# Optimization experiments

Hardware: AMD Instinct MI355X
Metric: run time of the kernel (lower is better)

## Reference

```python
import jax, jax.numpy as jnp
import numpy as np

B, N, PS = 8, 2048, 32
P = N // PS          # 64 patches
D, MLP, DEPTH, H, DH = 1024, 2048, 6, 8, 64
INNER = H * DH       # 512
K = 20
EPS = 1e-5


def setup_inputs() -> dict:
    key = jax.random.key(0)
    ks = jax.random.split(key, 16)
    r = lambda i, shape: jax.random.normal(ks[i], shape, dtype=jnp.float32) * 0.02
    return {
        "x": jax.random.normal(ks[0], (B, N, 3), dtype=jnp.float32),
        "x_pos_embed": r(1, (B, P + 1, D)),
        "w1": r(2, (64, 6)),   "g1": jnp.ones(64),  "b1": jnp.zeros(64),
        "w2": r(3, (64, 128)), "g2": jnp.ones(64),  "b2": jnp.zeros(64),
        "w3": r(4, (128, 128)),"g3": jnp.ones(128), "b3": jnp.zeros(128),
        "w4": r(5, (256, 256)),"g4": jnp.ones(256), "b4": jnp.zeros(256),
        "w5": r(6, (D, 512)),  "g5": jnp.ones(D),   "b5": jnp.zeros(D),
        "cls_token": r(7, (1, 1, D)),
        "ln1_g": jnp.ones((DEPTH, D)), "ln1_b": jnp.zeros((DEPTH, D)),
        "wqkv": r(8, (DEPTH, D, 3 * INNER)),
        "wout": r(9, (DEPTH, INNER, D)), "bout": jnp.zeros((DEPTH, D)),
        "ln2_g": jnp.ones((DEPTH, D)), "ln2_b": jnp.zeros((DEPTH, D)),
        "wff1": r(10, (DEPTH, D, MLP)), "bff1": jnp.zeros((DEPTH, MLP)),
        "wff2": r(11, (DEPTH, MLP, D)), "bff2": jnp.zeros((DEPTH, D)),
    }


def _knn(x, k):  # x: [B, C, N] -> neighbor idx [B, N, k]
    xx = jnp.sum(x * x, axis=1)                        # [B, N]
    inner = jnp.einsum('bcn,bcm->bnm', x, x)           # [B, N, N]
    dist = 2.0 * inner - xx[:, :, None] - xx[:, None, :]  # = -||xi-xj||^2
    return jax.lax.top_k(dist, k)[1]


def _graph_feature(x, k):  # x: [B, C, N] -> [B, N, k, 2C]
    idx = _knn(x, k)
    xt = jnp.transpose(x, (0, 2, 1))                   # [B, N, C]
    nbr = jax.vmap(lambda f, i: f[i])(xt, idx)         # gather: [B, N, k, C]
    ctr = jnp.broadcast_to(xt[:, :, None, :], nbr.shape)
    return jnp.concatenate([nbr - ctr, ctr], axis=-1)


def _leaky(v):
    return jnp.where(v >= 0, v, 0.2 * v)


def _edge_conv(x, w, g, b, k):  # EdgeConv block: graph feat -> 1x1 conv -> BN(train) -> lrelu -> max over k
    f = _graph_feature(x, k)                           # [B, N, k, 2C]
    y = jnp.einsum('bnkc,oc->bonk', f, w)              # [B, O, N, k]
    mu = jnp.mean(y, axis=(0, 2, 3), keepdims=True)
    var = jnp.var(y, axis=(0, 2, 3), keepdims=True)
    y = (y - mu) * jax.lax.rsqrt(var + EPS) * g[None, :, None, None] + b[None, :, None, None]
    return jnp.max(_leaky(y), axis=-1)                 # [B, O, N]


def _ln(x, g, b):
    mu = jnp.mean(x, axis=-1, keepdims=True)
    var = jnp.var(x, axis=-1, keepdims=True)
    return (x - mu) * jax.lax.rsqrt(var + EPS) * g + b


def reference(x, x_pos_embed, w1, g1, b1, w2, g2, b2, w3, g3, b3, w4, g4, b4,
              w5, g5, b5, cls_token, ln1_g, ln1_b, wqkv, wout, bout,
              ln2_g, ln2_b, wff1, bff1, wff2, bff2):
    scale = DH ** -0.5
    pts = jnp.transpose(x, (0, 2, 1))                  # [B, 3, N]
    x1 = _edge_conv(pts, w1, g1, b1, K)                # [B, 64, N]
    x2 = _edge_conv(x1, w2, g2, b2, K)                 # [B, 64, N]
    x3 = _edge_conv(x2, w3, g3, b3, K)                 # [B, 128, N]
    x4 = _edge_conv(x3, w4, g4, b4, K)                 # [B, 256, N]
    h = jnp.concatenate([x1, x2, x3, x4], axis=1)      # [B, 512, N]
    y = jnp.einsum('bcn,oc->bon', h, w5)               # conv5 1x1 -> [B, D, N]
    mu = jnp.mean(y, axis=(0, 2), keepdims=True)
    var = jnp.var(y, axis=(0, 2), keepdims=True)
    y = _leaky((y - mu) * jax.lax.rsqrt(var + EPS) * g5[None, :, None] + b5[None, :, None])
    # patch max-pool: 'b (p n) c -> (b p) n c' then max over n
    t = jnp.transpose(y, (0, 2, 1)).reshape(B * P, PS, D)
    t = jnp.max(t, axis=1).reshape(B, P, D)
    t = jnp.concatenate([jnp.broadcast_to(cls_token, (B, 1, D)), t], axis=1)  # [B, P+1, D]
    for i in range(DEPTH):
        t = t + x_pos_embed
        hn = _ln(t, ln1_g[i], ln1_b[i])
        qkv = (hn @ wqkv[i]).reshape(B, P + 1, 3, H, DH)
        q, k_, v = [jnp.transpose(qkv[:, :, j], (0, 2, 1, 3)) for j in range(3)]
        attn = jax.nn.softmax(jnp.einsum('bhld,bhmd->bhlm', q, k_) * scale, axis=-1)
        z = jnp.einsum('bhlm,bhmd->bhld', attn, v)
        z = jnp.transpose(z, (0, 2, 1, 3)).reshape(B, P + 1, INNER)
        t = t + z @ wout[i] + bout[i]
        hn = _ln(t, ln2_g[i], ln2_b[i])
        t = t + jax.nn.gelu(hn @ wff1[i] + bff1[i], approximate=False) @ wff2[i] + bff2[i]
    return t[:, 1:]                                    # [B, P, D]
```

## Files before the change

### kernel.cpp

```cpp
#include <hip/hip_runtime.h>
#include <math.h>

#define BB 8
#define NN 2048
#define PSZ 32
#define PP 64
#define DD 1024
#define MLPD 2048
#define DEPTH_ 6
#define HH 8
#define DHH 64
#define INNER_ 512
#define KK 20
#define TOK 65
#define EPSF 1e-5f

#define GEMM_ACC 1
#define GEMM_GELU 2
#define GEMM_OUTBF16 4

typedef __bf16 bf16_t;
typedef __attribute__((ext_vector_type(8))) __bf16 bf16x8;
typedef __attribute__((ext_vector_type(4))) float f32x4;

__global__ void transpose_x_kernel(const float* __restrict__ x, float* __restrict__ pts) {
    int gid = blockIdx.x * blockDim.x + threadIdx.x;
    if (gid >= BB * NN * 3) return;
    int c = gid % 3; int n = (gid / 3) % NN; int b = gid / (3 * NN);
    pts[(b * 3 + c) * NN + n] = x[gid];
}

__global__ void sqnorm_kernel(const float* __restrict__ x, int bs, int C, float* __restrict__ xx) {
    int gid = blockIdx.x * blockDim.x + threadIdx.x;
    if (gid >= BB * NN) return;
    int n = gid % NN; int b = gid / NN;
    const float* xp = x + b * bs + n;
    float s = 0.f;
    for (int c = 0; c < C; ++c) { float v = xp[c * NN]; s += v * v; }
    xx[gid] = s;
}

__global__ __launch_bounds__(256) void dist_kernel(const float* __restrict__ x, int bs, int C,
                                                   const float* __restrict__ xx, int b0,
                                                   float* __restrict__ dist) {
    __shared__ __align__(16) float As[16][132];
    __shared__ __align__(16) float Bs[16][132];
    int b = b0 + blockIdx.z;
    int n0 = blockIdx.y * 128, m0 = blockIdx.x * 128;
    int tid = threadIdx.x;
    int ty = tid >> 4, tx = tid & 15;
    float acc[2][2][4][4] = {};
    const float* xb = x + (long)b * bs;
    for (int k0 = 0; k0 < C; k0 += 16) {
        #pragma unroll
        for (int p = 0; p < 2; ++p) {
            int li = tid + p * 256;
            int i4 = li & 31;
            int kk = li >> 5;
            int c = k0 + kk;
            float4 va = make_float4(0.f, 0.f, 0.f, 0.f);
            float4 vb = va;
            if (c < C) {
                va = *(const float4*)&xb[(long)c * NN + n0 + i4 * 4];
                vb = *(const float4*)&xb[(long)c * NN + m0 + i4 * 4];
            }
            *(float4*)&As[kk][i4 * 4] = va;
            *(float4*)&Bs[kk][i4 * 4] = vb;
        }
        __syncthreads();
        #pragma unroll
        for (int kk = 0; kk < 16; ++kk) {
            float a[2][4], bv[2][4];
            *(float4*)a[0] = *(const float4*)&As[kk][ty * 4];
            *(float4*)a[1] = *(const float4*)&As[kk][64 + ty * 4];
            *(float4*)bv[0] = *(const float4*)&Bs[kk][tx * 4];
            *(float4*)bv[1] = *(const float4*)&Bs[kk][64 + tx * 4];
            #pragma unroll
            for (int ri = 0; ri < 2; ++ri)
                #pragma unroll
                for (int ci = 0; ci < 2; ++ci)
                    #pragma unroll
                    for (int i = 0; i < 4; ++i)
                        #pragma unroll
                        for (int j = 0; j < 4; ++j)
                            acc[ri][ci][i][j] += a[ri][i] * bv[ci][j];
        }
        __syncthreads();
    }
    float* db = dist + (long)blockIdx.z * NN * NN;
    const float* xxb = xx + b * NN;
    float xm[2][4];
    #pragma unroll
    for (int ci = 0; ci < 2; ++ci)
        #pragma unroll
        for (int j = 0; j < 4; ++j)
            xm[ci][j] = xxb[m0 + ci * 64 + tx * 4 + j];
    #pragma unroll
    for (int ri = 0; ri < 2; ++ri)
        #pragma unroll
        for (int i = 0; i < 4; ++i) {
            int n = n0 + ri * 64 + ty * 4 + i;
            float xn = xxb[n];
            #pragma unroll
            for (int ci = 0; ci < 2; ++ci) {
                int m = m0 + ci * 64 + tx * 4;
                float4 st;
                st.x = 2.f * acc[ri][ci][i][0] - xn - xm[ci][0];
                st.y = 2.f * acc[ri][ci][i][1] - xn - xm[ci][1];
                st.z = 2.f * acc[ri][ci][i][2] - xn - xm[ci][2];
                st.w = 2.f * acc[ri][ci][i][3] - xn - xm[ci][3];
                *(float4*)&db[(long)n * NN + m] = st;
            }
        }
}

__global__ __launch_bounds__(256) void topk_kernel(const float* __restrict__ dist, int b0,
                                                   int* __restrict__ idx) {
    __shared__ float cval[4][64];
    __shared__ int   cidx[4][64];
    int b = b0 + blockIdx.y;
    int wid = threadIdx.x >> 6, lane = threadIdx.x & 63;
    int n = blockIdx.x * 4 + wid;
    const float* row = dist + ((long)blockIdx.y * NN + n) * NN;
    float vals[32];
    #pragma unroll
    for (int s = 0; s < 32; ++s) vals[s] = row[s * 64 + lane];
    int* op = idx + ((long)b * NN + n) * KK;

    float lm = vals[0];
    #pragma unroll
    for (int s = 1; s < 32; ++s) lm = fmaxf(lm, vals[s]);

    float sv = lm;
    #pragma unroll
    for (int k = 2; k <= 64; k <<= 1) {
        #pragma unroll
        for (int j = k >> 1; j > 0; j >>= 1) {
            float pv = __shfl_xor(sv, j);
            bool lower = (lane & j) == 0;
            bool up = (lane & k) != 0;
            bool ownBetter = sv > pv;
            bool keepOwn = ownBetter ^ (lower == up);
            sv = keepOwn ? sv : pv;
        }
    }
    float t = __shfl(sv, 19);

    int base = 0;
    #pragma unroll
    for (int s = 0; s < 32; ++s) {
        bool q = vals[s] >= t;
        unsigned long long m = __ballot(q);
        int my = base + (int)__builtin_amdgcn_mbcnt_hi((unsigned)(m >> 32),
                         __builtin_amdgcn_mbcnt_lo((unsigned)m, 0u));
        if (q && my < 64) { cval[wid][my] = vals[s]; cidx[wid][my] = s * 64 + lane; }
        base += (int)__popcll(m);
    }
    __asm__ volatile("s_waitcnt lgkmcnt(0)" ::: "memory");

    if (base <= 64) {
        float v = (lane < base) ? cval[wid][lane] : -INFINITY;
        int   ii = (lane < base) ? cidx[wid][lane] : 0x7FFFFFFF;
        #pragma unroll
        for (int k = 2; k <= 64; k <<= 1) {
            #pragma unroll
            for (int j = k >> 1; j > 0; j >>= 1) {
                float pv = __shfl_xor(v, j);
                int   pi = __shfl_xor(ii, j);
                bool lower = (lane & j) == 0;
                bool up = (lane & k) != 0;
                bool ownBetter = (v > pv) || (v == pv && ii < pi);
                bool keepOwn = ownBetter ^ (lower == up);
                if (!keepOwn) { v = pv; ii = pi; }
            }
        }
        if (lane < KK) op[lane] = ii;
    } else {
        for (int kk = 0; kk < KK; ++kk) {
            float bv = vals[0]; int bsl = 0;
            #pragma unroll
            for (int s = 1; s < 32; ++s) if (vals[s] > bv) { bv = vals[s]; bsl = s; }
            int bm = bsl * 64 + lane;
            for (int off = 32; off; off >>= 1) {
                float ov = __shfl_xor(bv, off);
                int om = __shfl_xor(bm, off);
                if (ov > bv || (ov == bv && om < bm)) { bv = ov; bm = om; }
            }
            int wslot = bm >> 6, wlane = bm & 63;
            #pragma unroll
            for (int s = 0; s < 32; ++s)
                if (s == wslot) vals[s] = (lane == wlane) ? -INFINITY : vals[s];
            if (lane == 0) op[kk] = bm;
        }
    }
}

__global__ __launch_bounds__(256) void pq_kernel(const float* __restrict__ x, int bs, int C,
                                                 const float* __restrict__ w, int O,
                                                 float* __restrict__ p, float* __restrict__ q) {
    __shared__ float wT[256][33];
    __shared__ float xs[128][32];
    int b = blockIdx.z;
    int o0 = blockIdx.y * 32;
    int n0 = blockIdx.x * 32;
    int tid = threadIdx.x;
    for (int i = tid; i < 2 * C * 32; i += 256) {
        int c2 = i % (2 * C), o = i / (2 * C);
        wT[c2][o] = w[(o0 + o) * 2 * C + c2];
    }
    for (int i = tid; i < C * 32; i += 256) {
        int nl = i % 32, c = i / 32;
        xs[c][nl] = x[b * bs + c * NN + n0 + nl];
    }
    __syncthreads();
    int o_l = tid & 31;
    int n_base = (tid >> 5) * 4;
    float ps[4] = {0.f, 0.f, 0.f, 0.f};
    float qs[4] = {0.f, 0.f, 0.f, 0.f};
    for (int c = 0; c < C; ++c) {
        float4 xv = *(const float4*)&xs[c][n_base];
        float wa = wT[c][o_l];
        float wb = wT[C + c][o_l];
        float d = wb - wa;
        ps[0] += xv.x * wa; qs[0] += xv.x * d;
        ps[1] += xv.y * wa; qs[1] += xv.y * d;
        ps[2] += xv.z * wa; qs[2] += xv.z * d;
        ps[3] += xv.w * wa; qs[3] += xv.w * d;
    }
    for (int j = 0; j < 4; ++j) {
        long r = (long)(b * NN + n0 + n_base + j) * O + o0 + o_l;
        p[r] = ps[j];
        q[r] = qs[j];
    }
}

__global__ void zero_stats_kernel(double* __restrict__ s1, double* __restrict__ s2) {
    int t = blockIdx.x * blockDim.x + threadIdx.x;
    if (t < 1024) { s1[t] = 0.0; s2[t] = 0.0; }
}

__global__ __launch_bounds__(256) void edge_stats_kernel(const float* __restrict__ p, const float* __restrict__ q,
                                                         const int* __restrict__ idx, int O,
                                                         double* __restrict__ gsum, double* __restrict__ gsumsq) {
    int tid = threadIdx.x;
    int o = tid % O;
    int grp = tid / O;
    int ngrp = 256 / O;
    int rows_per_blk = (BB * NN) / gridDim.x;
    int r0 = blockIdx.x * rows_per_blk;
    double s = 0.0, ss = 0.0;
    for (int r = r0 + grp; r < r0 + rows_per_blk; r += ngrp) {
        int b = r / NN;
        float qv = q[r * O + o];
        for (int k = 0; k < KK; ++k) {
            int j = idx[r * KK + k];
            float v = p[(b * NN + j) * O + o] + qv;
            s += v; ss += (double)v * v;
        }
    }
    atomicAdd(&gsum[o], s);
    atomicAdd(&gsumsq[o], ss);
}

__global__ void bn_finalize_kernel(const double* __restrict__ gsum, const double* __restrict__ gsumsq,
                                   const float* __restrict__ g, const float* __restrict__ bb, int O, double cnt,
                                   float* __restrict__ scale, float* __restrict__ shift) {
    int o = blockIdx.x * blockDim.x + threadIdx.x;
    if (o >= O) return;
    double mean = gsum[o] / cnt;
    double var = gsumsq[o] / cnt - mean * mean;
    float inv = rsqrtf((float)var + EPSF);
    float sc = g[o] * inv;
    scale[o] = sc;
    shift[o] = bb[o] - (float)mean * sc;
}

__global__ void edge_out_kernel(const float* __restrict__ p, const float* __restrict__ q,
                                const int* __restrict__ idx, int O,
                                const float* __restrict__ scale, const float* __restrict__ shift,
                                float* __restrict__ out, int obs) {
    int gid = blockIdx.x * blockDim.x + threadIdx.x;
    if (gid >= BB * NN * O) return;
    int o = gid % O; int n = (gid / O) % NN; int b = gid / (O * NN);
    int r = b * NN + n;
    float qv = q[r * O + o];
    float sc = scale[o], sh = shift[o];
    float m = -INFINITY;
    for (int k = 0; k < KK; ++k) {
        int j = idx[r * KK + k];
        float v = (p[(b * NN + j) * O + o] + qv) * sc + sh;
        v = (v >= 0.f) ? v : 0.2f * v;
        m = fmaxf(m, v);
    }
    out[b * obs + o * NN + n] = m;
}

__global__ __launch_bounds__(256) void transpose_cvt_kernel(const float* __restrict__ in,
                                                            bf16_t* __restrict__ outp,
                                                            int R, int C, long s_in, long s_out) {
    __shared__ float tile[32][33];
    const float* ib = in + (long)blockIdx.z * s_in;
    bf16_t* ob = outp + (long)blockIdx.z * s_out;
    int r0 = blockIdx.y * 32, c0 = blockIdx.x * 32;
    int tx = threadIdx.x & 31, tg = threadIdx.x >> 5;
    for (int i = 0; i < 4; ++i) {
        int r = tg + i * 8;
        tile[r][tx] = ib[(long)(r0 + r) * C + c0 + tx];
    }
    __syncthreads();
    for (int i = 0; i < 4; ++i) {
        int c = tg + i * 8;
        ob[(long)(c0 + c) * R + r0 + tx] = (bf16_t)tile[tx][c];
    }
}

__global__ __launch_bounds__(256) void gemm_bf16_kernel(const float* __restrict__ A,
                                                        const bf16_t* __restrict__ Bt,
                                                        const float* __restrict__ bias,
                                                        float* __restrict__ out,
                                                        int M, int Kd, int Nd,
                                                        long sA, long sBt, long sO, int flags) {
    __shared__ __align__(16) bf16_t As[64 * 32];
    __shared__ __align__(16) bf16_t Bs[64 * 32];
    const float* Ab = A + (long)blockIdx.z * sA;
    const bf16_t* Bb = Bt + (long)blockIdx.z * sBt;
    int row0 = blockIdx.y * 64, col0 = blockIdx.x * 64;
    int tid = threadIdx.x;
    int lane = tid & 63, wv = tid >> 6;
    int wm = wv >> 1, wn = wv & 1;
    int srow = tid >> 2;
    int skp = (tid & 3) * 8;
    f32x4 acc[2][2] = {};
    for (int k0 = 0; k0 < Kd; k0 += 32) {
        {
            int r = row0 + srow;
            float av[8];
            if (r < M) {
                const float* ap = Ab + (long)r * Kd + k0 + skp;
                float4 a0 = *(const float4*)ap;
                float4 a1 = *(const float4*)(ap + 4);
                av[0] = a0.x; av[1] = a0.y; av[2] = a0.z; av[3] = a0.w;
                av[4] = a1.x; av[5] = a1.y; av[6] = a1.z; av[7] = a1.w;
            } else {
                #pragma unroll
                for (int j = 0; j < 8; ++j) av[j] = 0.f;
            }
            bf16x8 v;
            #pragma unroll
            for (int j = 0; j < 8; ++j) v[j] = (bf16_t)av[j];
            *(bf16x8*)&As[((skp >> 3) * 64 + srow) * 8] = v;
        }
        {
            const bf16_t* bp = Bb + (long)(col0 + srow) * Kd + k0 + skp;
            bf16x8 v = *(const bf16x8*)bp;
            *(bf16x8*)&Bs[((skp >> 3) * 64 + srow) * 8] = v;
        }
        __syncthreads();
        int q = lane >> 4, cl = lane & 15;
        bf16x8 a0v = *(const bf16x8*)&As[(q * 64 + wm * 32 + cl) * 8];
        bf16x8 a1v = *(const bf16x8*)&As[(q * 64 + wm * 32 + 16 + cl) * 8];
        bf16x8 b0v = *(const bf16x8*)&Bs[(q * 64 + wn * 32 + cl) * 8];
        bf16x8 b1v = *(const bf16x8*)&Bs[(q * 64 + wn * 32 + 16 + cl) * 8];
        acc[0][0] = __builtin_amdgcn_mfma_f32_16x16x32_bf16(a0v, b0v, acc[0][0], 0, 0, 0);
        acc[0][1] = __builtin_amdgcn_mfma_f32_16x16x32_bf16(a0v, b1v, acc[0][1], 0, 0, 0);
        acc[1][0] = __builtin_amdgcn_mfma_f32_16x16x32_bf16(a1v, b0v, acc[1][0], 0, 0, 0);
        acc[1][1] = __builtin_amdgcn_mfma_f32_16x16x32_bf16(a1v, b1v, acc[1][1], 0, 0, 0);
        __syncthreads();
    }
    int q = lane >> 4, cl = lane & 15;
    float* Obf = out + (long)blockIdx.z * sO;
    bf16_t* Obh = (bf16_t*)out + (long)blockIdx.z * sO;
    for (int mt = 0; mt < 2; ++mt)
        for (int nt = 0; nt < 2; ++nt)
            #pragma unroll
            for (int r = 0; r < 4; ++r) {
                int row = row0 + wm * 32 + mt * 16 + q * 4 + r;
                if (row >= M) continue;
                int col = col0 + wn * 32 + nt * 16 + cl;
                float v = acc[mt][nt][r];
                if (bias) v += bias[col];
                if (flags & GEMM_GELU) v = 0.5f * v * (1.f + erff(v * 0.70710678118654752f));
                long oidx = (long)row * Nd + col;
                if (flags & GEMM_OUTBF16) Obh[oidx] = (bf16_t)v;
                else if (flags & GEMM_ACC) Obf[oidx] += v;
                else Obf[oidx] = v;
            }
}

__global__ __launch_bounds__(256) void gemm_kernel(const float* __restrict__ A, const float* __restrict__ Bm,
                                                   const float* __restrict__ bias, float* __restrict__ out,
                                                   int M, int Kd, int Nd, long sA, long sB, long sO, int flags) {
    __shared__ float As[16][65];
    __shared__ float Bs[16][64];
    const float* Ab = A + (long)blockIdx.z * sA;
    const float* Bb = Bm + (long)blockIdx.z * sB;
    float* Ob = out + (long)blockIdx.z * sO;
    int row0 = blockIdx.y * 64, col0 = blockIdx.x * 64;
    int tid = threadIdx.x;
    int ty = tid / 16, tx = tid % 16;
    float acc[4][4] = {};
    for (int k0 = 0; k0 < Kd; k0 += 16) {
        for (int i = 0; i < 4; ++i) {
            int li = tid + i * 256;
            int m = li / 16, kk = li % 16;
            int r = row0 + m;
            As[kk][m] = (r < M) ? Ab[(long)r * Kd + k0 + kk] : 0.f;
        }
        for (int i = 0; i < 4; ++i) {
            int li = tid + i * 256;
            int kk = li / 64, n = li % 64;
            int c = col0 + n;
            Bs[kk][n] = (c < Nd) ? Bb[(long)(k0 + kk) * Nd + c] : 0.f;
        }
        __syncthreads();
        for (int kk = 0; kk < 16; ++kk) {
            float a[4], bv[4];
            for (int i = 0; i < 4; ++i) a[i] = As[kk][ty * 4 + i];
            for (int j = 0; j < 4; ++j) bv[j] = Bs[kk][tx * 4 + j];
            for (int i = 0; i < 4; ++i)
                for (int j = 0; j < 4; ++j)
                    acc[i][j] += a[i] * bv[j];
        }
        __syncthreads();
    }
    for (int i = 0; i < 4; ++i) {
        int r = row0 + ty * 4 + i;
        if (r >= M) continue;
        for (int j = 0; j < 4; ++j) {
            int c = col0 + tx * 4 + j;
            if (c >= Nd) continue;
            float v = acc[i][j];
            if (bias) v += bias[c];
            if (flags & GEMM_GELU) v = 0.5f * v * (1.f + erff(v * 0.70710678118654752f));
            long oidx = (long)r * Nd + c;
            if (flags & GEMM_ACC) Ob[oidx] += v; else Ob[oidx] = v;
        }
    }
}

__global__ __launch_bounds__(256) void bn5_stats_bf16_kernel(const bf16_t* __restrict__ y5,
                                                             const float* __restrict__ g,
                                                             const float* __restrict__ bb,
                                                             float* __restrict__ scale, float* __restrict__ shift) {
    __shared__ double ssum[256], ssq[256];
    int d = blockIdx.x;
    int tid = threadIdx.x;
    double s = 0.0, sq = 0.0;
    for (int b = 0; b < BB; ++b) {
        const bf16_t* row = y5 + ((long)b * DD + d) * NN;
        for (int n = tid; n < NN; n += 256) { float v = (float)row[n]; s += v; sq += (double)v * v; }
    }
    ssum[tid] = s; ssq[tid] = sq;
    __syncthreads();
    for (int st = 128; st > 0; st >>= 1) {
        if (tid < st) { ssum[tid] += ssum[tid + st]; ssq[tid] += ssq[tid + st]; }
        __syncthreads();
    }
    if (tid == 0) {
        double cnt = (double)BB * NN;
        double mean = ssum[0] / cnt;
        double var = ssq[0] / cnt - mean * mean;
        float inv = rsqrtf((float)var + EPSF);
        float sc = g[d] * inv;
        scale[d] = sc;
        shift[d] = bb[d] - (float)mean * sc;
    }
}

__global__ __launch_bounds__(256) void bn5_stats_kernel(const float* __restrict__ y5, const float* __restrict__ g,
                                                        const float* __restrict__ bb,
                                                        float* __restrict__ scale, float* __restrict__ shift) {
    __shared__ double ssum[256], ssq[256];
    int d = blockIdx.x;
    int tid = threadIdx.x;
    double s = 0.0, sq = 0.0;
    for (int b = 0; b < BB; ++b) {
        const float* row = y5 + ((long)b * DD + d) * NN;
        for (int n = tid; n < NN; n += 256) { float v = row[n]; s += v; sq += (double)v * v; }
    }
    ssum[tid] = s; ssq[tid] = sq;
    __syncthreads();
    for (int st = 128; st > 0; st >>= 1) {
        if (tid < st) { ssum[tid] += ssum[tid + st]; ssq[tid] += ssq[tid + st]; }
        __syncthreads();
    }
    if (tid == 0) {
        double cnt = (double)BB * NN;
        double mean = ssum[0] / cnt;
        double var = ssq[0] / cnt - mean * mean;
        float inv = rsqrtf((float)var + EPSF);
        float sc = g[d] * inv;
        scale[d] = sc;
        shift[d] = bb[d] - (float)mean * sc;
    }
}

__global__ void pool_bf16_kernel(const bf16_t* __restrict__ y5, const float* __restrict__ scale,
                                 const float* __restrict__ shift, const float* __restrict__ cls,
                                 float* __restrict__ t) {
    int gid = blockIdx.x * blockDim.x + threadIdx.x;
    if (gid >= BB * TOK * DD) return;
    int d = gid % DD; int l = (gid / DD) % TOK; int b = gid / (DD * TOK);
    float v;
    if (l == 0) {
        v = cls[d];
    } else {
        int pp = l - 1;
        const bf16_t* row = y5 + ((long)b * DD + d) * NN + pp * PSZ;
        float sc = scale[d], sh = shift[d];
        float m = -INFINITY;
        for (int i = 0; i < PSZ; ++i) {
            float u = (float)row[i] * sc + sh;
            u = (u >= 0.f) ? u : 0.2f * u;
            m = fmaxf(m, u);
        }
        v = m;
    }
    t[gid] = v;
}

__global__ void pool_kernel(const float* __restrict__ y5, const float* __restrict__ scale,
                            const float* __restrict__ shift, const float* __restrict__ cls,
                            float* __restrict__ t) {
    int gid = blockIdx.x * blockDim.x + threadIdx.x;
    if (gid >= BB * TOK * DD) return;
    int d = gid % DD; int l = (gid / DD) % TOK; int b = gid / (DD * TOK);
    float v;
    if (l == 0) {
        v = cls[d];
    } else {
        int pp = l - 1;
        const float* row = y5 + ((long)b * DD + d) * NN + pp * PSZ;
        float sc = scale[d], sh = shift[d];
        float m = -INFINITY;
        for (int i = 0; i < PSZ; ++i) {
            float u = row[i] * sc + sh;
            u = (u >= 0.f) ? u : 0.2f * u;
            m = fmaxf(m, u);
        }
        v = m;
    }
    t[gid] = v;
}

__global__ __launch_bounds__(256) void ln_kernel(float* __restrict__ t, const float* __restrict__ pos,
                                                 const float* __restrict__ g, const float* __restrict__ bb,
                                                 float* __restrict__ hn, int addpos) {
    __shared__ double s1[256], s2[256];
    long r = blockIdx.x;
    int tid = threadIdx.x;
    float vals[4];
    double s = 0.0, sq = 0.0;
    for (int i = 0; i < 4; ++i) {
        int d = tid + i * 256;
        float v = t[r * DD + d];
        if (addpos) { v += pos[r * DD + d]; t[r * DD + d] = v; }
        vals[i] = v; s += v; sq += (double)v * v;
    }
    s1[tid] = s; s2[tid] = sq;
    __syncthreads();
    for (int st = 128; st > 0; st >>= 1) {
        if (tid < st) { s1[tid] += s1[tid + st]; s2[tid] += s2[tid + st]; }
        __syncthreads();
    }
    double mean = s1[0] / DD;
    float var = (float)(s2[0] / DD - mean * mean);
    float fm = (float)mean;
    float inv = rsqrtf(var + EPSF);
    for (int i = 0; i < 4; ++i) {
        int d = tid + i * 256;
        hn[r * DD + d] = (vals[i] - fm) * inv * g[d] + bb[d];
    }
}

__global__ __launch_bounds__(256) void attn_kernel(const float* __restrict__ qkv, float* __restrict__ z) {
    __shared__ float ks[TOK][DHH + 1];
    __shared__ float vs[TOK][DHH + 1];
    __shared__ float ss[TOK][TOK];
    int bh = blockIdx.x;
    int b = bh / HH, h = bh % HH;
    int tid = threadIdx.x;
    for (int i = tid; i < TOK * DHH; i += 256) {
        int l = i / DHH, d = i % DHH;
        long base = (long)(b * TOK + l) * 1536;
        ks[l][d] = qkv[base + 512 + h * DHH + d];
        vs[l][d] = qkv[base + 1024 + h * DHH + d];
    }
    __syncthreads();
    for (int i = tid; i < TOK * TOK; i += 256) {
        int l = i / TOK, m = i % TOK;
        const float* qrow = qkv + (long)(b * TOK + l) * 1536 + h * DHH;
        float acc = 0.f;
        for (int d = 0; d < DHH; ++d) acc += qrow[d] * ks[m][d];
        ss[l][m] = acc * 0.125f;
    }
    __syncthreads();
    if (tid < TOK) {
        float mx = -INFINITY;
        for (int m = 0; m < TOK; ++m) mx = fmaxf(mx, ss[tid][m]);
        float sum = 0.f;
        for (int m = 0; m < TOK; ++m) { float e = expf(ss[tid][m] - mx); ss[tid][m] = e; sum += e; }
        float invs = 1.f / sum;
        for (int m = 0; m < TOK; ++m) ss[tid][m] *= invs;
    }
    __syncthreads();
    for (int i = tid; i < TOK * DHH; i += 256) {
        int l = i / DHH, d = i % DHH;
        float acc = 0.f;
        for (int m = 0; m < TOK; ++m) acc += ss[l][m] * vs[m][d];
        z[(long)(b * TOK + l) * INNER_ + h * DHH + d] = acc;
    }
}

__global__ void final_kernel(const float* __restrict__ t, float* __restrict__ out) {
    int gid = blockIdx.x * blockDim.x + threadIdx.x;
    if (gid >= BB * PP * DD) return;
    int d = gid % DD; int p = (gid / DD) % PP; int b = gid / (DD * PP);
    out[gid] = t[((long)b * TOK + 1 + p) * DD + d];
}

static inline int ceil_div(long a, long b) { return (int)((a + b - 1) / b); }

extern "C" void kernel_launch(void* const* d_in, const int* in_sizes, int n_in,
                              void* d_out, int out_size, void* d_ws, size_t ws_size,
                              hipStream_t stream) {
    const float* x    = (const float*)d_in[0];
    const float* pos  = (const float*)d_in[1];
    const float* w1   = (const float*)d_in[2];
    const float* g1   = (const float*)d_in[3];
    const float* b1   = (const float*)d_in[4];
    const float* w2   = (const float*)d_in[5];
    const float* g2   = (const float*)d_in[6];
    const float* b2   = (const float*)d_in[7];
    const float* w3   = (const float*)d_in[8];
    const float* g3   = (const float*)d_in[9];
    const float* b3   = (const float*)d_in[10];
    const float* w4   = (const float*)d_in[11];
    const float* g4   = (const float*)d_in[12];
    const float* b4   = (const float*)d_in[13];
    const float* w5   = (const float*)d_in[14];
    const float* g5   = (const float*)d_in[15];
    const float* b5   = (const float*)d_in[16];
    const float* cls  = (const float*)d_in[17];
    const float* ln1g = (const float*)d_in[18];
    const float* ln1b = (const float*)d_in[19];
    const float* wqkv = (const float*)d_in[20];
    const float* wout = (const float*)d_in[21];
    const float* bout = (const float*)d_in[22];
    const float* ln2g = (const float*)d_in[23];
    const float* ln2b = (const float*)d_in[24];
    const float* wff1 = (const float*)d_in[25];
    const float* bff1 = (const float*)d_in[26];
    const float* wff2 = (const float*)d_in[27];
    const float* bff2 = (const float*)d_in[28];
    float* out = (float*)d_out;

    char* ws = (char*)d_ws;
    size_t off = 0;
    auto alloc = [&](size_t bytes) -> char* {
        char* ptr = ws + off;
        off = (off + bytes + 255) & ~(size_t)255;
        return ptr;
    };
    float*  h      = (float*)alloc((size_t)BB * 512 * NN * 4);
    float*  t      = (float*)alloc((size_t)BB * TOK * DD * 4);
    float*  hn     = (float*)alloc((size_t)BB * TOK * DD * 4);
    float*  qkvb   = (float*)alloc((size_t)BB * TOK * 1536 * 4);
    float*  zb     = (float*)alloc((size_t)BB * TOK * INNER_ * 4);
    float*  ub     = (float*)alloc((size_t)BB * TOK * MLPD * 4);
    double* dsum   = (double*)alloc(1024 * 8);
    double* dsq    = (double*)alloc(1024 * 8);
    float*  scaleb = (float*)alloc(1024 * 4);
    float*  shiftb = (float*)alloc(1024 * 4);
    size_t ubase = off;

    size_t uoff = ubase;
    auto ualloc = [&](size_t bytes) -> char* {
        char* ptr = ws + uoff;
        uoff = (uoff + bytes + 255) & ~(size_t)255;
        return ptr;
    };
    float* pts  = (float*)ualloc((size_t)BB * 3 * NN * 4);
    float* xx   = (float*)ualloc((size_t)BB * NN * 4);
    int*   idxb = (int*)  ualloc((size_t)BB * NN * KK * 4);
    float* pbuf = (float*)ualloc((size_t)BB * NN * 256 * 4);
    float* qbuf = (float*)ualloc((size_t)BB * NN * 256 * 4);
    size_t dist_rel = uoff - ubase;
    float* distb = (float*)(ws + uoff);

    size_t voff = ubase;
    auto valloc = [&](size_t bytes) -> char* {
        char* ptr = ws + voff;
        voff = (voff + bytes + 255) & ~(size_t)255;
        return ptr;
    };
    bf16_t* hT     = (bf16_t*)valloc((size_t)BB * NN * 512 * 2);
    bf16_t* wTqkv  = (bf16_t*)valloc((size_t)DEPTH_ * 1536 * DD * 2);
    bf16_t* wTout  = (bf16_t*)valloc((size_t)DEPTH_ * DD * INNER_ * 2);
    bf16_t* wTff1  = (bf16_t*)valloc((size_t)DEPTH_ * MLPD * DD * 2);
    bf16_t* wTff2  = (bf16_t*)valloc((size_t)DEPTH_ * DD * MLPD * 2);
    size_t stage_bf16 = voff - ubase;

    size_t conv_full  = dist_rel + (size_t)BB * NN * NN * 4;
    size_t conv_batch = dist_rel + (size_t)NN * NN * 4;
    size_t stage_fp32 = (size_t)BB * DD * NN * 4;

    auto mx = [](size_t a, size_t b) { return a > b ? a : b; };
    bool use_bf16 = ws_size >= ubase + mx(conv_batch, stage_bf16);
    bool full     = ws_size >= ubase + mx(conv_full, use_bf16 ? stage_bf16 : stage_fp32);
    if (!use_bf16 && ws_size < ubase + mx(conv_batch, stage_fp32)) return;
    bf16_t* y5bf = (bf16_t*)h;
    float*  y5f  = (float*)(ws + ubase);

    transpose_x_kernel<<<ceil_div((long)BB * NN * 3, 256), 256, 0, stream>>>(x, pts);

    auto run_conv = [&](const float* xin, int xbs, int C, const float* w,
                        const float* g, const float* bb, float* hout, int O) {
        sqnorm_kernel<<<ceil_div((long)BB * NN, 256), 256, 0, stream>>>(xin, xbs, C, xx);
        if (full) {
            dist_kernel<<<dim3(NN / 128, NN / 128, BB), 256, 0, stream>>>(xin, xbs, C, xx, 0, distb);
            topk_kernel<<<dim3(NN / 4, BB), 256, 0, stream>>>(distb, 0, idxb);
        } else {
            for (int b = 0; b < BB; ++b) {
                dist_kernel<<<dim3(NN / 128, NN / 128, 1), 256, 0, stream>>>(xin, xbs, C, xx, b, distb);
                topk_kernel<<<dim3(NN / 4, 1), 256, 0, stream>>>(distb, b, idxb);
            }
        }
        {
            dim3 grid(NN / 32, O / 32, BB);
            pq_kernel<<<grid, 256, 0, stream>>>(xin, xbs, C, w, O, pbuf, qbuf);
        }
        zero_stats_kernel<<<4, 256, 0, stream>>>(dsum, dsq);
        edge_stats_kernel<<<256, 256, 0, stream>>>(pbuf, qbuf, idxb, O, dsum, dsq);
        bn_finalize_kernel<<<1, 256, 0, stream>>>(dsum, dsq, g, bb, O, (double)BB * NN * KK, scaleb, shiftb);
        edge_out_kernel<<<ceil_div((long)BB * NN * O, 256), 256, 0, stream>>>(
            pbuf, qbuf, idxb, O, scaleb, shiftb, hout, 512 * NN);
    };
    run_conv(pts, 3 * NN, 3, w1, g1, b1, h, 64);
    run_conv(h, 512 * NN, 64, w2, g2, b2, h + 64 * NN, 64);
    run_conv(h + 64 * NN, 512 * NN, 64, w3, g3, b3, h + 128 * NN, 128);
    run_conv(h + 128 * NN, 512 * NN, 128, w4, g4, b4, h + 256 * NN, 256);

    const int M = BB * TOK;
    if (use_bf16) {
        transpose_cvt_kernel<<<dim3(NN / 32, 512 / 32, BB), 256, 0, stream>>>(
            h, hT, 512, NN, (long)512 * NN, (long)NN * 512);
        transpose_cvt_kernel<<<dim3(1536 / 32, DD / 32, DEPTH_), 256, 0, stream>>>(
            wqkv, wTqkv, DD, 1536, (long)DD * 1536, (long)1536 * DD);
        transpose_cvt_kernel<<<dim3(DD / 32, INNER_ / 32, DEPTH_), 256, 0, stream>>>(
            wout, wTout, INNER_, DD, (long)INNER_ * DD, (long)DD * INNER_);
        transpose_cvt_kernel<<<dim3(MLPD / 32, DD / 32, DEPTH_), 256, 0, stream>>>(
            wff1, wTff1, DD, MLPD, (long)DD * MLPD, (long)MLPD * DD);
        transpose_cvt_kernel<<<dim3(DD / 32, MLPD / 32, DEPTH_), 256, 0, stream>>>(
            wff2, wTff2, MLPD, DD, (long)MLPD * DD, (long)DD * MLPD);

        gemm_bf16_kernel<<<dim3(NN / 64, DD / 64, BB), 256, 0, stream>>>(
            w5, hT, nullptr, (float*)y5bf, DD, 512, NN, 0L, (long)NN * 512, (long)DD * NN, GEMM_OUTBF16);
        bn5_stats_bf16_kernel<<<DD, 256, 0, stream>>>(y5bf, g5, b5, scaleb, shiftb);
        pool_bf16_kernel<<<ceil_div((long)BB * TOK * DD, 256), 256, 0, stream>>>(y5bf, scaleb, shiftb, cls, t);

        for (int i = 0; i < DEPTH_; ++i) {
            ln_kernel<<<M, 256, 0, stream>>>(t, pos, ln1g + i * DD, ln1b + i * DD, hn, 1);
            gemm_bf16_kernel<<<dim3(1536 / 64, ceil_div(M, 64), 1), 256, 0, stream>>>(
                hn, wTqkv + (size_t)i * 1536 * DD, nullptr, qkvb, M, DD, 1536, 0L, 0L, 0L, 0);
            attn_kernel<<<BB * HH, 256, 0, stream>>>(qkvb, zb);
            gemm_bf16_kernel<<<dim3(DD / 64, ceil_div(M, 64), 1), 256, 0, stream>>>(
                zb, wTout + (size_t)i * DD * INNER_, bout + i * DD, t, M, INNER_, DD, 0L, 0L, 0L, GEMM_ACC);
            ln_kernel<<<M, 256, 0, stream>>>(t, nullptr, ln2g + i * DD, ln2b + i * DD, hn, 0);
            gemm_bf16_kernel<<<dim3(MLPD / 64, ceil_div(M, 64), 1), 256, 0, stream>>>(
                hn, wTff1 + (size_t)i * MLPD * DD, bff1 + i * MLPD, ub, M, DD, MLPD, 0L, 0L, 0L, GEMM_GELU);
            gemm_bf16_kernel<<<dim3(DD / 64, ceil_div(M, 64), 1), 256, 0, stream>>>(
                ub, wTff2 + (size_t)i * DD * MLPD, bff2 + i * DD, t, M, MLPD, DD, 0L, 0L, 0L, GEMM_ACC);
        }
    } else {
        gemm_kernel<<<dim3(NN / 64, DD / 64, BB), 256, 0, stream>>>(
            w5, h, nullptr, y5f, DD, 512, NN, 0L, (long)512 * NN, (long)DD * NN, 0);
        bn5_stats_kernel<<<DD, 256, 0, stream>>>(y5f, g5, b5, scaleb, shiftb);
        pool_kernel<<<ceil_div((long)BB * TOK * DD, 256), 256, 0, stream>>>(y5f, scaleb, shiftb, cls, t);
        for (int i = 0; i < DEPTH_; ++i) {
            ln_kernel<<<M, 256, 0, stream>>>(t, pos, ln1g + i * DD, ln1b + i * DD, hn, 1);
            gemm_kernel<<<dim3(1536 / 64, ceil_div(M, 64), 1), 256, 0, stream>>>(
                hn, wqkv + (size_t)i * DD * 1536, nullptr, qkvb, M, DD, 1536, 0L, 0L, 0L, 0);
            attn_kernel<<<BB * HH, 256, 0, stream>>>(qkvb, zb);
            gemm_kernel<<<dim3(DD / 64, ceil_div(M, 64), 1), 256, 0, stream>>>(
                zb, wout + (size_t)i * INNER_ * DD, bout + i * DD, t, M, INNER_, DD, 0L, 0L, 0L, GEMM_ACC);
            ln_kernel<<<M, 256, 0, stream>>>(t, nullptr, ln2g + i * DD, ln2b + i * DD, hn, 0);
            gemm_kernel<<<dim3(MLPD / 64, ceil_div(M, 64), 1), 256, 0, stream>>>(
                hn, wff1 + (size_t)i * DD * MLPD, bff1 + i * MLPD, ub, M, DD, MLPD, 0L, 0L, 0L, GEMM_GELU);
            gemm_kernel<<<dim3(DD / 64, ceil_div(M, 64), 1), 256, 0, stream>>>(
                ub, wff2 + (size_t)i * MLPD * DD, bff2 + i * DD, t, M, MLPD, DD, 0L, 0L, 0L, GEMM_ACC);
        }
    }

    final_kernel<<<ceil_div((long)BB * PP * DD, 256), 256, 0, stream>>>(t, out);
}
```

Before: 2.039 ms.

## Exploit distance matrix symmetry by computing upper-triangle tiles and writing transposes

The pairwise distance kernel now launches only the 136 upper-triangular 128x128 tiles per batch instead of all 256. Each off-diagonal tile also writes its transpose, staged through shared memory in four 32-row slices. This roughly halves the GEMM arithmetic and the reads of the input features. The full matrix is still written to global memory, so write traffic stays the same. It adds extra synchronisation and a serial loop that maps a block index to its tile.

```diff
diff --git a/kernel.cpp b/kernel.cpp
--- a/kernel.cpp
+++ b/kernel.cpp
@@ -43,10 +43,18 @@
 __global__ __launch_bounds__(256) void dist_kernel(const float* __restrict__ x, int bs, int C,
                                                    const float* __restrict__ xx, int b0,
                                                    float* __restrict__ dist) {
-    __shared__ __align__(16) float As[16][132];
-    __shared__ __align__(16) float Bs[16][132];
+    __shared__ __align__(16) float smem[4224];
+    float (*As)[132] = (float(*)[132])smem;
+    float (*Bs)[132] = (float(*)[132])(smem + 16 * 132);
+    float (*tb)[132] = (float(*)[132])smem;
+
+    int q = blockIdx.x;
+    int bi = 0, rem = q;
+    while (rem >= (16 - bi)) { rem -= (16 - bi); ++bi; }
+    int bj = bi + rem;
+
     int b = b0 + blockIdx.z;
-    int n0 = blockIdx.y * 128, m0 = blockIdx.x * 128;
+    int n0 = bi * 128, m0 = bj * 128;
     int tid = threadIdx.x;
     int ty = tid >> 4, tx = tid & 15;
     float acc[2][2][4][4] = {};
@@ -99,19 +107,49 @@
     for (int ri = 0; ri < 2; ++ri)
         #pragma unroll
         for (int i = 0; i < 4; ++i) {
+            float xn = xxb[n0 + ri * 64 + ty * 4 + i];
+            #pragma unroll
+            for (int ci = 0; ci < 2; ++ci)
+                #pragma unroll
+                for (int j = 0; j < 4; ++j)
+                    acc[ri][ci][i][j] = 2.f * acc[ri][ci][i][j] - xn - xm[ci][j];
+        }
+    #pragma unroll
+    for (int ri = 0; ri < 2; ++ri)
+        #pragma unroll
+        for (int i = 0; i < 4; ++i) {
             int n = n0 + ri * 64 + ty * 4 + i;
-            float xn = xxb[n];
             #pragma unroll
-            for (int ci = 0; ci < 2; ++ci) {
-                int m = m0 + ci * 64 + tx * 4;
-                float4 st;
-                st.x = 2.f * acc[ri][ci][i][0] - xn - xm[ci][0];
-                st.y = 2.f * acc[ri][ci][i][1] - xn - xm[ci][1];
-                st.z = 2.f * acc[ri][ci][i][2] - xn - xm[ci][2];
-                st.w = 2.f * acc[ri][ci][i][3] - xn - xm[ci][3];
-                *(float4*)&db[(long)n * NN + m] = st;
+            for (int ci = 0; ci < 2; ++ci)
+                *(float4*)&db[(long)n * NN + m0 + ci * 64 + tx * 4] = *(float4*)&acc[ri][ci][i][0];
+        }
+    if (bi != bj) {
+        #pragma unroll
+        for (int s = 0; s < 4; ++s) {
+            __syncthreads();
+            int ci = s >> 1;
+            if ((tx >> 3) == (s & 1)) {
+                #pragma unroll
+                for (int ri = 0; ri < 2; ++ri)
+                    #pragma unroll
+                    for (int j = 0; j < 4; ++j) {
+                        float4 v;
+                        v.x = acc[ri][ci][0][j];
+                        v.y = acc[ri][ci][1][j];
+                        v.z = acc[ri][ci][2][j];
+                        v.w = acc[ri][ci][3][j];
+                        *(float4*)&tb[(tx & 7) * 4 + j][ri * 64 + ty * 4] = v;
+                    }
             }
-        }
+            __syncthreads();
+            int r = tid >> 3;
+            int c0 = (tid & 7) * 16;
+            long orow = (long)(m0 + s * 32 + r) * NN + n0 + c0;
+            #pragma unroll
+            for (int c4 = 0; c4 < 4; ++c4)
+                *(float4*)&db[orow + c4 * 4] = *(const float4*)&tb[r][c0 + c4 * 4];
+        }
+    }
 }
 
 __global__ __launch_bounds__(256) void topk_kernel(const float* __restrict__ dist, int b0,
@@ -714,15 +752,16 @@
 
     transpose_x_kernel<<<ceil_div((long)BB * NN * 3, 256), 256, 0, stream>>>(x, pts);
 
+    const int NTRI = 136;
     auto run_conv = [&](const float* xin, int xbs, int C, const float* w,
                         const float* g, const float* bb, float* hout, int O) {
         sqnorm_kernel<<<ceil_div((long)BB * NN, 256), 256, 0, stream>>>(xin, xbs, C, xx);
         if (full) {
-            dist_kernel<<<dim3(NN / 128, NN / 128, BB), 256, 0, stream>>>(xin, xbs, C, xx, 0, distb);
+            dist_kernel<<<dim3(NTRI, 1, BB), 256, 0, stream>>>(xin, xbs, C, xx, 0, distb);
             topk_kernel<<<dim3(NN / 4, BB), 256, 0, stream>>>(distb, 0, idxb);
         } else {
             for (int b = 0; b < BB; ++b) {
-                dist_kernel<<<dim3(NN / 128, NN / 128, 1), 256, 0, stream>>>(xin, xbs, C, xx, b, distb);
+                dist_kernel<<<dim3(NTRI, 1, 1), 256, 0, stream>>>(xin, xbs, C, xx, b, distb);
                 topk_kernel<<<dim3(NN / 4, 1), 256, 0, stream>>>(distb, b, idxb);
             }
         }
```

Measured after the change: 2.018 ms. Within noise of the previous version (-1.0%).
